# Performance work log

Measured on AMD Instinct MI355X. Metric: run time of the kernel, lower is better.

The kernel has to match this reference:

```python
import jax, jax.numpy as jnp
import numpy as np

N = 50000      # ncount
IN_CH = 256    # in_channels
OUT_CH = 128   # out_channels
NNZ = 800000   # nnz per sparse matrix (avg degree 16)


def _spmm(rows, cols, vals, dense, n_rows):
    # sparse(COO) @ dense : gather rows of dense by col index, scale, scatter-add by row
    contrib = vals[:, None] * dense[cols]              # [nnz, F]
    return jax.ops.segment_sum(contrib, rows, num_segments=n_rows)


def setup_inputs() -> dict:
    key = jax.random.key(0)
    ks = jax.random.split(key, 12)
    phi_indices = jnp.stack([
        jax.random.randint(ks[0], (NNZ,), 0, N),
        jax.random.randint(ks[1], (NNZ,), 0, N)])
    phi_values = jax.random.normal(ks[2], (NNZ,), dtype=jnp.float32)
    phi_inverse_indices = jnp.stack([
        jax.random.randint(ks[3], (NNZ,), 0, N),
        jax.random.randint(ks[4], (NNZ,), 0, N)])
    phi_inverse_values = jax.random.normal(ks[5], (NNZ,), dtype=jnp.float32)
    feature_indices = jnp.stack([
        jax.random.randint(ks[6], (NNZ,), 0, N),       # node index
        jax.random.randint(ks[7], (NNZ,), 0, IN_CH)])  # feature column
    feature_values = jax.random.normal(ks[8], (NNZ,), dtype=jnp.float32)
    # xavier_uniform for weight_matrix
    limit = float(np.sqrt(6.0 / (IN_CH + OUT_CH)))
    weight_matrix = jax.random.uniform(ks[9], (IN_CH, OUT_CH), jnp.float32, -limit, limit)
    # diagonal filter Theta init uniform(0.9, 1.1)
    diagonal_weight_filter = jax.random.uniform(ks[10], (N,), jnp.float32, 0.9, 1.1)
    return {
        "phi_indices": phi_indices,
        "phi_values": phi_values,
        "phi_inverse_indices": phi_inverse_indices,
        "phi_inverse_values": phi_inverse_values,
        "feature_indices": feature_indices,
        "feature_values": feature_values,
        "weight_matrix": weight_matrix,
        "diagonal_weight_filter": diagonal_weight_filter,
        "dropout": 0,
    }


def reference(phi_indices, phi_values, phi_inverse_indices, phi_inverse_values,
              feature_indices, feature_values, weight_matrix,
              diagonal_weight_filter, dropout):
    # rescaled_phi = phi @ diag(theta): scales column j of phi by theta[j]
    scaled_phi_vals = phi_values * diagonal_weight_filter[phi_indices[1]]
    # filtered = features(sparse N x IN) @ W  -> [N, OUT]
    filtered = _spmm(feature_indices[0], feature_indices[1], feature_values,
                     weight_matrix, N)
    # (phi * D * phi_inv) @ filtered computed associatively without dense N x N:
    tmp = _spmm(phi_inverse_indices[0], phi_inverse_indices[1],
                phi_inverse_values, filtered, N)              # phi_inv @ filtered
    localized = _spmm(phi_indices[0], phi_indices[1],
                      scaled_phi_vals, tmp, N)                # (phi D) @ tmp
    # dropout in eval mode (training=False) is identity
    return jax.nn.relu(localized)
```

## Files before the change

kernel.cpp:

```cpp
#include <hip/hip_runtime.h>
#include <hip/hip_fp16.h>


#define OUT_CH 128
#define HALF_CH 64
#define RPB 256
#define RPB_SHIFT 8
#define MAX_NB 256
#define EPB 4096
#define EPT_C 8
#define STAGE_CAP 8192


__global__ __launch_bounds__(512) void bucket_hist_kernel(
    const int* __restrict__ rows0, int n0,
    const int* __restrict__ rows1, int n1,
    const int* __restrict__ rows2, int n2,
    int* __restrict__ hist_part,
    int NB, int NBLK)
{
    int m = blockIdx.y;
    const int* rows = (m == 0) ? rows0 : (m == 1) ? rows1 : rows2;
    int nnz         = (m == 0) ? n0    : (m == 1) ? n1    : n2;
    __shared__ int bins[MAX_NB];
    int t = threadIdx.x;
    if (t < NB) bins[t] = 0;
    __syncthreads();
    int base = blockIdx.x * EPB;
    #pragma unroll
    for (int k = 0; k < EPB / 512; ++k) {
        int i = base + k * 512 + t;
        if (i < nnz) atomicAdd(&bins[rows[i] >> RPB_SHIFT], 1);
    }
    __syncthreads();
    int* out = hist_part + ((size_t)(m * NBLK + blockIdx.x)) * NB;
    if (t < NB) out[t] = bins[t];
}


__global__ __launch_bounds__(256) void reduce_totals_kernel(
    const int* __restrict__ hist_part, int* __restrict__ totals, int NB, int NBLK)
{
    int w = blockIdx.x * 4 + (threadIdx.x >> 6);
    if (w >= 3 * NB) return;
    int lane = threadIdx.x & 63;
    int m = w / NB, b = w - m * NB;
    const int* hp = hist_part + (size_t)m * NBLK * NB + b;
    int sum = 0;
    for (int blk = lane; blk < NBLK; blk += 64)
        sum += hp[(size_t)blk * NB];
    #pragma unroll
    for (int s = 1; s < 64; s <<= 1) sum += __shfl_xor(sum, s);
    if (lane == 0) totals[w] = sum;
}


__global__ __launch_bounds__(256) void scan_bases_kernel(
    const int* __restrict__ totals, int* __restrict__ bases,
    int* __restrict__ cursor, int NB)
{
    int m = blockIdx.x, t = threadIdx.x;
    int x = (t < NB) ? totals[m * NB + t] : 0;
    int lane = t & 63, wid = t >> 6;
    int incl = x;
    #pragma unroll
    for (int s = 1; s < 64; s <<= 1) {
        int y = __shfl_up(incl, s);
        if (lane >= s) incl += y;
    }
    __shared__ int wtot[4], wbase[4];
    if (lane == 63) wtot[wid] = incl;
    __syncthreads();
    if (t == 0) {
        int run = 0;
        #pragma unroll
        for (int w = 0; w < 4; ++w) { int v = wtot[w]; wbase[w] = run; run += v; }
    }
    __syncthreads();
    if (t < NB) {
        int excl = wbase[wid] + incl - x;
        bases[m * NB + t] = excl;
        cursor[m * NB + t] = excl;
    }
}


__global__ __launch_bounds__(512) void bucket_scatter_kernel(
    const int* __restrict__ rows0, const int* __restrict__ cols0, const float* __restrict__ vals0, int n0,
    const int* __restrict__ rows1, const int* __restrict__ cols1, const float* __restrict__ vals1, int n1,
    const int* __restrict__ rows2, const int* __restrict__ cols2, const float* __restrict__ vals2, int n2,
    const float* __restrict__ theta,
    const int* __restrict__ hist_part, int* __restrict__ cursor,
    int2* __restrict__ eb0, int2* __restrict__ eb1, int2* __restrict__ eb2,
    int NB, int NBLK)
{
    int m = blockIdx.y;
    const int* rows; const int* cols; const float* vals; int nnz; int2* eb;
    if (m == 0)      { rows = rows0; cols = cols0; vals = vals0; nnz = n0; eb = eb0; }
    else if (m == 1) { rows = rows1; cols = cols1; vals = vals1; nnz = n1; eb = eb1; }
    else             { rows = rows2; cols = cols2; vals = vals2; nnz = n2; eb = eb2; }

    __shared__ int2 staged[EPB];
    __shared__ unsigned char bucket_of[EPB];
    __shared__ int lstart[MAX_NB];
    __shared__ int lcur[MAX_NB];
    __shared__ int gbase[MAX_NB];
    __shared__ int wtot[8], wbase[8];

    int t = threadIdx.x;
    int base = blockIdx.x * EPB;
    bool fold = (m == 2);

    int  bk[EPT_C];
    int2 pl[EPT_C];
    #pragma unroll
    for (int k = 0; k < EPT_C; ++k) {
        int i = base + k * 512 + t;
        if (i < nnz) {
            int r = rows[i], c = cols[i];
            float v = vals[i];
            if (fold) v *= theta[c];
            bk[k] = r >> RPB_SHIFT;
            pl[k] = make_int2(c | ((r & (RPB - 1)) << 16), __float_as_int(v));
        } else bk[k] = -1;
    }

    {
        const int* hp = hist_part + ((size_t)(m * NBLK + blockIdx.x)) * NB;
        int lh = (t < NB) ? hp[t] : 0;
        int lane = t & 63, wid = t >> 6;
        int incl = lh;
        #pragma unroll
        for (int s = 1; s < 64; s <<= 1) {
            int y = __shfl_up(incl, s);
            if (lane >= s) incl += y;
        }
        if (lane == 63) wtot[wid] = incl;
        __syncthreads();
        if (t == 0) {
            int run = 0;
            #pragma unroll
            for (int w = 0; w < 8; ++w) { int v = wtot[w]; wbase[w] = run; run += v; }
        }
        __syncthreads();
        if (t < NB) {
            int excl = wbase[wid] + incl - lh;
            lstart[t] = excl;
            lcur[t]   = excl;
            gbase[t] = atomicAdd(&cursor[m * NB + t], lh);
        }
    }
    __syncthreads();

    #pragma unroll
    for (int k = 0; k < EPT_C; ++k) {
        if (bk[k] >= 0) {
            int idx = atomicAdd(&lcur[bk[k]], 1);
            staged[idx] = pl[k];
            bucket_of[idx] = (unsigned char)bk[k];
        }
    }
    __syncthreads();

    int count = min(EPB, nnz - base);
    for (int i = t; i < count; i += 512) {
        int b = bucket_of[i];
        int dest = gbase[b] + (i - lstart[b]);
        eb[dest] = staged[i];
    }
}


__global__ __launch_bounds__(512) void bucket_to_csr_kernel(
    const int2* __restrict__ eb0, const int2* __restrict__ eb1, const int2* __restrict__ eb2,
    unsigned int* __restrict__ ec0, unsigned int* __restrict__ ec1, unsigned int* __restrict__ ec2,
    const int* __restrict__ bases,
    int* __restrict__ off,
    int n0, int n1, int n2, int NB, int n)
{
    int m = blockIdx.y;
    int b = blockIdx.x;
    const int2* eb; unsigned int* ec; int nnz;
    if (m == 0)      { eb = eb0; ec = ec0; nnz = n0; }
    else if (m == 1) { eb = eb1; ec = ec1; nnz = n1; }
    else             { eb = eb2; ec = ec2; nnz = n2; }
    int base = bases[m * NB + b];
    int end  = (b + 1 < NB) ? bases[m * NB + b + 1] : nnz;
    int cnt  = end - base;

    __shared__ unsigned int staged_c[STAGE_CAP];
    __shared__ int hist[RPB];
    __shared__ int cur[RPB];
    __shared__ int loc[RPB + 1];
    __shared__ int wtot[4];
    __shared__ int wbase[4];
    int t = threadIdx.x;
    if (t < RPB) { hist[t] = 0; cur[t] = 0; }
    __syncthreads();
    for (int i = base + t; i < end; i += 512)
        atomicAdd(&hist[(eb[i].x >> 16) & (RPB - 1)], 1);
    __syncthreads();
    {
        int x = (t < RPB) ? hist[t] : 0;
        int lane = t & 63, wid = t >> 6;
        int incl = x;
        #pragma unroll
        for (int s = 1; s < 64; s <<= 1) {
            int y = __shfl_up(incl, s);
            if (lane >= s) incl += y;
        }
        if (lane == 63 && wid < 4) wtot[wid] = incl;
        __syncthreads();
        if (t == 0) {
            int run = 0;
            #pragma unroll
            for (int w = 0; w < 4; ++w) { int v = wtot[w]; wbase[w] = run; run += v; }
        }
        __syncthreads();
        if (t < RPB) {
            loc[t] = wbase[wid] + incl - x;
            if (t == RPB - 1) loc[RPB] = wbase[3] + incl;
        }
    }
    __syncthreads();
    if (t < RPB) {
        int r = b * RPB + t;
        if (r <= n) off[(size_t)m * (n + 1) + r] = base + loc[t];
        if (b == NB - 1 && t == 0) off[(size_t)m * (n + 1) + n] = nnz;
    }
    if (cnt <= STAGE_CAP) {
        for (int i = base + t; i < end; i += 512) {
            int2 e = eb[i];
            int rl = (e.x >> 16) & (RPB - 1);
            int rk = atomicAdd(&cur[rl], 1);
            unsigned short h = __half_as_ushort(__float2half_rn(__int_as_float(e.y)));
            staged_c[loc[rl] + rk] = (unsigned int)(e.x & 0xFFFF) | ((unsigned int)h << 16);
        }
        __syncthreads();
        for (int i = t; i < cnt; i += 512)
            ec[base + i] = staged_c[i];
    } else {
        for (int i = base + t; i < end; i += 512) {
            int2 e = eb[i];
            int rl = (e.x >> 16) & (RPB - 1);
            int rk = atomicAdd(&cur[rl], 1);
            unsigned short h = __half_as_ushort(__float2half_rn(__int_as_float(e.y)));
            ec[base + loc[rl] + rk] = (unsigned int)(e.x & 0xFFFF) | ((unsigned int)h << 16);
        }
    }
}


template<bool SRC_H, bool DST_H, bool RELU>
__global__ __launch_bounds__(256) void spmm_csr_kernel(
    const int* __restrict__ off, const unsigned int* __restrict__ edges,
    const void* __restrict__ dense_v, void* __restrict__ out_v, int nrows)
{
    int lane = threadIdx.x & 63;
    int r = blockIdx.x * 4 + (threadIdx.x >> 6);
    if (r >= nrows) return;
    int j   = __builtin_amdgcn_readfirstlane(off[r]);
    int end = __builtin_amdgcn_readfirstlane(off[r + 1]);
    const float2*  df = (const float2*)dense_v;
    const __half2* dh = (const __half2*)dense_v;

    float2 a0 = make_float2(0.f, 0.f), a1 = make_float2(0.f, 0.f);

    for (; j + 16 <= end; j += 16) {
        unsigned int e[16]; float2 d[16];
        #pragma unroll
        for (int k = 0; k < 16; ++k) e[k] = edges[j + k];
        #pragma unroll
        for (int k = 0; k < 16; ++k) {
            if (SRC_H) d[k] = __half22float2(dh[(size_t)(e[k] & 0xFFFF) * HALF_CH + lane]);
            else       d[k] = df[(size_t)(e[k] & 0xFFFF) * HALF_CH + lane];
        }
        #pragma unroll
        for (int k = 0; k < 16; ++k) {
            float v = __half2float(__ushort_as_half((unsigned short)(e[k] >> 16)));
            if (k & 1) { a1.x = fmaf(v, d[k].x, a1.x); a1.y = fmaf(v, d[k].y, a1.y); }
            else       { a0.x = fmaf(v, d[k].x, a0.x); a0.y = fmaf(v, d[k].y, a0.y); }
        }
    }
    for (; j + 8 <= end; j += 8) {
        unsigned int e[8]; float2 d[8];
        #pragma unroll
        for (int k = 0; k < 8; ++k) e[k] = edges[j + k];
        #pragma unroll
        for (int k = 0; k < 8; ++k) {
            if (SRC_H) d[k] = __half22float2(dh[(size_t)(e[k] & 0xFFFF) * HALF_CH + lane]);
            else       d[k] = df[(size_t)(e[k] & 0xFFFF) * HALF_CH + lane];
        }
        #pragma unroll
        for (int k = 0; k < 8; ++k) {
            float v = __half2float(__ushort_as_half((unsigned short)(e[k] >> 16)));
            if (k & 1) { a1.x = fmaf(v, d[k].x, a1.x); a1.y = fmaf(v, d[k].y, a1.y); }
            else       { a0.x = fmaf(v, d[k].x, a0.x); a0.y = fmaf(v, d[k].y, a0.y); }
        }
    }
    for (; j + 4 <= end; j += 4) {
        unsigned int e[4]; float2 d[4];
        #pragma unroll
        for (int k = 0; k < 4; ++k) e[k] = edges[j + k];
        #pragma unroll
        for (int k = 0; k < 4; ++k) {
            if (SRC_H) d[k] = __half22float2(dh[(size_t)(e[k] & 0xFFFF) * HALF_CH + lane]);
            else       d[k] = df[(size_t)(e[k] & 0xFFFF) * HALF_CH + lane];
        }
        #pragma unroll
        for (int k = 0; k < 4; ++k) {
            float v = __half2float(__ushort_as_half((unsigned short)(e[k] >> 16)));
            if (k & 1) { a1.x = fmaf(v, d[k].x, a1.x); a1.y = fmaf(v, d[k].y, a1.y); }
            else       { a0.x = fmaf(v, d[k].x, a0.x); a0.y = fmaf(v, d[k].y, a0.y); }
        }
    }
    for (; j < end; ++j) {
        unsigned int e0 = edges[j];
        float2 d0;
        if (SRC_H) d0 = __half22float2(dh[(size_t)(e0 & 0xFFFF) * HALF_CH + lane]);
        else       d0 = df[(size_t)(e0 & 0xFFFF) * HALF_CH + lane];
        float v0 = __half2float(__ushort_as_half((unsigned short)(e0 >> 16)));
        a0.x = fmaf(v0, d0.x, a0.x); a0.y = fmaf(v0, d0.y, a0.y);
    }
    float2 res = make_float2(a0.x + a1.x, a0.y + a1.y);
    if (RELU) { res.x = fmaxf(res.x, 0.f); res.y = fmaxf(res.y, 0.f); }
    if (DST_H) ((__half2*)out_v)[(size_t)r * HALF_CH + lane] = __float22half2_rn(res);
    else       ((float2*) out_v)[(size_t)r * HALF_CH + lane] = res;
}


__global__ __launch_bounds__(256) void spmm_atomic_kernel(
    const int* __restrict__ rows, const int* __restrict__ cols,
    const float* __restrict__ vals, const float* __restrict__ theta,
    const float* __restrict__ dense, float* __restrict__ out, int nnz)
{
    int idx = blockIdx.x * blockDim.x + threadIdx.x;
    int e = idx >> 7;
    int f = idx & (OUT_CH - 1);
    if (e >= nnz) return;
    int r = rows[e];
    int c = cols[e];
    float v = vals[e];
    if (theta != nullptr) v *= theta[c];
    atomicAdd(&out[(size_t)r * OUT_CH + f], v * dense[(size_t)c * OUT_CH + f]);
}

__global__ __launch_bounds__(256) void relu_kernel(float* __restrict__ out, int n4)
{
    int i = blockIdx.x * blockDim.x + threadIdx.x;
    if (i >= n4) return;
    float4 v = ((float4*)out)[i];
    v.x = fmaxf(v.x, 0.f); v.y = fmaxf(v.y, 0.f);
    v.z = fmaxf(v.z, 0.f); v.w = fmaxf(v.w, 0.f);
    ((float4*)out)[i] = v;
}


static inline size_t align16(size_t x) { return (x + 15) & ~(size_t)15; }

extern "C" void kernel_launch(void* const* d_in, const int* in_sizes, int n_in,
                              void* d_out, int out_size, void* d_ws, size_t ws_size,
                              hipStream_t stream)
{
    const int*   phi_idx   = (const int*)d_in[0];
    const float* phi_vals  = (const float*)d_in[1];
    const int*   phii_idx  = (const int*)d_in[2];
    const float* phii_vals = (const float*)d_in[3];
    const int*   feat_idx  = (const int*)d_in[4];
    const float* feat_vals = (const float*)d_in[5];
    const float* W         = (const float*)d_in[6];
    const float* theta     = (const float*)d_in[7];

    const int nnz_phi  = in_sizes[1];
    const int nnz_phii = in_sizes[3];
    const int nnz_feat = in_sizes[5];
    const int n_nodes  = in_sizes[7];
    const int in_ch    = in_sizes[6] / OUT_CH;
    const size_t dense_elems = (size_t)n_nodes * OUT_CH;
    const long long total_e = (long long)nnz_feat + nnz_phii + nnz_phi;

    const int NB = (n_nodes + RPB - 1) >> RPB_SHIFT;
    int max_nnz = nnz_feat > nnz_phii ? nnz_feat : nnz_phii;
    if (nnz_phi > max_nnz) max_nnz = nnz_phi;
    const int NBLK = (max_nnz + EPB - 1) / EPB;

    size_t p = 0;
    size_t filtered_off = p; p += align16(dense_elems * sizeof(__half));
    size_t tmp_off      = p; p += align16(dense_elems * sizeof(__half));
    size_t off_off      = p; p += align16((size_t)3 * (n_nodes + 1) * sizeof(int));
    size_t hp_off       = p; p += align16((size_t)3 * NBLK * NB * sizeof(int));
    size_t tot_off      = p; p += align16((size_t)3 * NB * sizeof(int));
    size_t bas_off      = p; p += align16((size_t)3 * NB * sizeof(int));
    size_t cur_off      = p; p += align16((size_t)3 * NB * sizeof(int));
    size_t eb_off       = p; p += align16((size_t)total_e * sizeof(int2));
    size_t ec_off       = p; p += align16((size_t)total_e * sizeof(unsigned int));
    size_t need = p;

    char* ws = (char*)d_ws;
    dim3 block256(256);
    dim3 block512(512);

    bool fast_ok = (ws_size >= need) && (NB <= MAX_NB) && (n_nodes <= 65536) &&
                   (in_ch <= 65536);

    if (fast_ok) {
        __half* filtered = (__half*)(ws + filtered_off);
        __half* tmp      = (__half*)(ws + tmp_off);
        int* off_arr    = (int*)(ws + off_off);
        int* hist_part  = (int*)(ws + hp_off);
        int* totals     = (int*)(ws + tot_off);
        int* bases      = (int*)(ws + bas_off);
        int* cursor     = (int*)(ws + cur_off);
        int2* eb0 = (int2*)(ws + eb_off);
        int2* eb1 = eb0 + nnz_feat;
        int2* eb2 = eb1 + nnz_phii;
        unsigned int* ec0 = (unsigned int*)(ws + ec_off);
        unsigned int* ec1 = ec0 + nnz_feat;
        unsigned int* ec2 = ec1 + nnz_phii;

        const int* rows0 = feat_idx;  const int* cols0 = feat_idx + nnz_feat;
        const int* rows1 = phii_idx;  const int* cols1 = phii_idx + nnz_phii;
        const int* rows2 = phi_idx;   const int* cols2 = phi_idx  + nnz_phi;

        bucket_hist_kernel<<<dim3(NBLK, 3), block512, 0, stream>>>(
            rows0, nnz_feat, rows1, nnz_phii, rows2, nnz_phi,
            hist_part, NB, NBLK);

        int nwaves = 3 * NB;
        reduce_totals_kernel<<<dim3((nwaves + 3) / 4), block256, 0, stream>>>(
            hist_part, totals, NB, NBLK);

        scan_bases_kernel<<<dim3(3), block256, 0, stream>>>(
            totals, bases, cursor, NB);

        bucket_scatter_kernel<<<dim3(NBLK, 3), block512, 0, stream>>>(
            rows0, cols0, feat_vals, nnz_feat,
            rows1, cols1, phii_vals, nnz_phii,
            rows2, cols2, phi_vals,  nnz_phi,
            theta, hist_part, cursor, eb0, eb1, eb2, NB, NBLK);

        bucket_to_csr_kernel<<<dim3(NB, 3), block512, 0, stream>>>(
            eb0, eb1, eb2, ec0, ec1, ec2, bases, off_arr,
            nnz_feat, nnz_phii, nnz_phi, NB, n_nodes);

        int* off_f  = off_arr;
        int* off_pi = off_arr + (n_nodes + 1);
        int* off_p  = off_arr + 2 * (n_nodes + 1);

        dim3 grid_r((unsigned)((n_nodes + 3) / 4));
        spmm_csr_kernel<false, true, false><<<grid_r, block256, 0, stream>>>(
            off_f,  ec0, (const void*)W, (void*)filtered, n_nodes);
        spmm_csr_kernel<true, true, false><<<grid_r, block256, 0, stream>>>(
            off_pi, ec1, (const void*)filtered, (void*)tmp, n_nodes);
        spmm_csr_kernel<true, false, true><<<grid_r, block256, 0, stream>>>(
            off_p,  ec2, (const void*)tmp, d_out, n_nodes);
    } else {
        float* filtered = (float*)ws;
        float* tmp      = filtered + dense_elems;
        hipMemsetAsync(filtered, 0, 2 * dense_elems * sizeof(float), stream);
        hipMemsetAsync(d_out, 0, (size_t)out_size * sizeof(float), stream);
        {
            long long t = (long long)nnz_feat * OUT_CH;
            spmm_atomic_kernel<<<dim3((unsigned)((t + 255) / 256)), block256, 0, stream>>>(
                feat_idx, feat_idx + nnz_feat, feat_vals, nullptr, W, filtered, nnz_feat);
        }
        {
            long long t = (long long)nnz_phii * OUT_CH;
            spmm_atomic_kernel<<<dim3((unsigned)((t + 255) / 256)), block256, 0, stream>>>(
                phii_idx, phii_idx + nnz_phii, phii_vals, nullptr, filtered, tmp, nnz_phii);
        }
        {
            long long t = (long long)nnz_phi * OUT_CH;
            spmm_atomic_kernel<<<dim3((unsigned)((t + 255) / 256)), block256, 0, stream>>>(
                phi_idx, phi_idx + nnz_phi, phi_vals, theta, tmp, (float*)d_out, nnz_phi);
        }
        {
            int n4 = out_size / 4;
            relu_kernel<<<dim3((n4 + 255) / 256), block256, 0, stream>>>((float*)d_out, n4);
        }
    }
}
```

Baseline: 209.2 us.

## Fuse bucket histogram and scatter into one block-local sort pass

Replaces the separate histogram and global-scatter kernels with a single kernel that reads the COO input once, sorts each block's edges by bucket in shared memory, and writes them contiguously along with per-block bucket offsets. The CSR builder then gathers each bucket's segments from every source block instead of reading a pre-scattered global buffer. Values are converted to half early, and metadata and values are split into separate arrays, which shrinks intermediate traffic. The cost is a second read of the input that is removed, traded against more fragmented segment reads in the CSR kernel and a new limit on the block count.

```diff
diff --git a/kernel.cpp b/kernel.cpp
--- a/kernel.cpp
+++ b/kernel.cpp
@@ -7,34 +7,102 @@
 #define RPB 256
 #define RPB_SHIFT 8
 #define MAX_NB 256
+#define MAX_NBLK 256
 #define EPB 4096
 #define EPT_C 8
 #define STAGE_CAP 8192
 
 
-__global__ __launch_bounds__(512) void bucket_hist_kernel(
-    const int* __restrict__ rows0, int n0,
-    const int* __restrict__ rows1, int n1,
-    const int* __restrict__ rows2, int n2,
+__global__ __launch_bounds__(512) void sort_local_kernel(
+    const int* __restrict__ rows0, const int* __restrict__ cols0, const float* __restrict__ vals0, int n0,
+    const int* __restrict__ rows1, const int* __restrict__ cols1, const float* __restrict__ vals1, int n1,
+    const int* __restrict__ rows2, const int* __restrict__ cols2, const float* __restrict__ vals2, int n2,
+    const float* __restrict__ theta,
     int* __restrict__ hist_part,
+    unsigned int*  __restrict__ ebm0, unsigned int*  __restrict__ ebm1, unsigned int*  __restrict__ ebm2,
+    unsigned short* __restrict__ ebv0, unsigned short* __restrict__ ebv1, unsigned short* __restrict__ ebv2,
     int NB, int NBLK)
 {
     int m = blockIdx.y;
-    const int* rows = (m == 0) ? rows0 : (m == 1) ? rows1 : rows2;
-    int nnz         = (m == 0) ? n0    : (m == 1) ? n1    : n2;
-    __shared__ int bins[MAX_NB];
+    const int* rows; const int* cols; const float* vals; int nnz;
+    unsigned int* ebm; unsigned short* ebv;
+    if (m == 0)      { rows = rows0; cols = cols0; vals = vals0; nnz = n0; ebm = ebm0; ebv = ebv0; }
+    else if (m == 1) { rows = rows1; cols = cols1; vals = vals1; nnz = n1; ebm = ebm1; ebv = ebv1; }
+    else             { rows = rows2; cols = cols2; vals = vals2; nnz = n2; ebm = ebm2; ebv = ebv2; }
+
+    __shared__ unsigned int  staged_m[EPB];
+    __shared__ unsigned short staged_v[EPB];
+    __shared__ int lhist[MAX_NB];
+    __shared__ int lcur[MAX_NB];
+    __shared__ int wtot[8], wbase[8];
+
     int t = threadIdx.x;
-    if (t < NB) bins[t] = 0;
-    __syncthreads();
     int base = blockIdx.x * EPB;
+    bool fold = (m == 2);
+
+    if (t < NB) lhist[t] = 0;
+    __syncthreads();
+
+    int bk[EPT_C];
+    unsigned int  mt[EPT_C];
+    unsigned short vl[EPT_C];
     #pragma unroll
-    for (int k = 0; k < EPB / 512; ++k) {
+    for (int k = 0; k < EPT_C; ++k) {
         int i = base + k * 512 + t;
-        if (i < nnz) atomicAdd(&bins[rows[i] >> RPB_SHIFT], 1);
-    }
-    __syncthreads();
-    int* out = hist_part + ((size_t)(m * NBLK + blockIdx.x)) * NB;
-    if (t < NB) out[t] = bins[t];
+        if (i < nnz) {
+            int r = rows[i], c = cols[i];
+            float v = vals[i];
+            if (fold) v *= theta[c];
+            bk[k] = r >> RPB_SHIFT;
+            mt[k] = (unsigned int)c | ((unsigned int)(r & (RPB - 1)) << 16);
+            vl[k] = __half_as_ushort(__float2half_rn(v));
+            atomicAdd(&lhist[bk[k]], 1);
+        } else bk[k] = -1;
+    }
+    __syncthreads();
+
+    {
+        int x = (t < NB) ? lhist[t] : 0;
+        int lane = t & 63, wid = t >> 6;
+        int incl = x;
+        #pragma unroll
+        for (int s = 1; s < 64; s <<= 1) {
+            int y = __shfl_up(incl, s);
+            if (lane >= s) incl += y;
+        }
+        if (lane == 63) wtot[wid] = incl;
+        __syncthreads();
+        if (t == 0) {
+            int run = 0;
+            #pragma unroll
+            for (int w = 0; w < 8; ++w) { int v = wtot[w]; wbase[w] = run; run += v; }
+        }
+        __syncthreads();
+        int* out = hist_part + ((size_t)(m * NBLK + blockIdx.x)) * (NB + 1);
+        if (t < NB) {
+            int excl = wbase[wid] + incl - x;
+            lcur[t] = excl;
+            out[t] = excl;
+        }
+        if (t == 0) out[NB] = min(EPB, nnz - base);
+    }
+    __syncthreads();
+
+    #pragma unroll
+    for (int k = 0; k < EPT_C; ++k) {
+        if (bk[k] >= 0) {
+            int idx = atomicAdd(&lcur[bk[k]], 1);
+            staged_m[idx] = mt[k];
+            staged_v[idx] = vl[k];
+        }
+    }
+    __syncthreads();
+
+    int count = min(EPB, nnz - base);
+    for (int i = t; i < count; i += 512) {
+        ebm[base + i] = staged_m[i];
+        ebv[base + i] = staged_v[i];
+    }
 }
 
 
@@ -45,10 +113,12 @@
     if (w >= 3 * NB) return;
     int lane = threadIdx.x & 63;
     int m = w / NB, b = w - m * NB;
-    const int* hp = hist_part + (size_t)m * NBLK * NB + b;
+    const int* hp = hist_part + (size_t)m * NBLK * (NB + 1);
     int sum = 0;
-    for (int blk = lane; blk < NBLK; blk += 64)
-        sum += hp[(size_t)blk * NB];
+    for (int blk = lane; blk < NBLK; blk += 64) {
+        const int* row = hp + (size_t)blk * (NB + 1);
+        sum += row[b + 1] - row[b];
+    }
     #pragma unroll
     for (int s = 1; s < 64; s <<= 1) sum += __shfl_xor(sum, s);
     if (lane == 0) totals[w] = sum;
@@ -56,8 +126,7 @@
 
 
 __global__ __launch_bounds__(256) void scan_bases_kernel(
-    const int* __restrict__ totals, int* __restrict__ bases,
-    int* __restrict__ cursor, int NB)
+    const int* __restrict__ totals, int* __restrict__ bases, int NB)
 {
     int m = blockIdx.x, t = threadIdx.x;
     int x = (t < NB) ? totals[m * NB + t] : 0;
@@ -77,175 +146,131 @@
         for (int w = 0; w < 4; ++w) { int v = wtot[w]; wbase[w] = run; run += v; }
     }
     __syncthreads();
-    if (t < NB) {
-        int excl = wbase[wid] + incl - x;
-        bases[m * NB + t] = excl;
-        cursor[m * NB + t] = excl;
-    }
-}
-
-
-__global__ __launch_bounds__(512) void bucket_scatter_kernel(
-    const int* __restrict__ rows0, const int* __restrict__ cols0, const float* __restrict__ vals0, int n0,
-    const int* __restrict__ rows1, const int* __restrict__ cols1, const float* __restrict__ vals1, int n1,
-    const int* __restrict__ rows2, const int* __restrict__ cols2, const float* __restrict__ vals2, int n2,
-    const float* __restrict__ theta,
-    const int* __restrict__ hist_part, int* __restrict__ cursor,
-    int2* __restrict__ eb0, int2* __restrict__ eb1, int2* __restrict__ eb2,
-    int NB, int NBLK)
+    if (t < NB) bases[m * NB + t] = wbase[wid] + incl - x;
+}
+
+
+__global__ __launch_bounds__(512) void bucket_to_csr_kernel(
+    const unsigned int* __restrict__ ebm0, const unsigned int* __restrict__ ebm1, const unsigned int* __restrict__ ebm2,
+    const unsigned short* __restrict__ ebv0, const unsigned short* __restrict__ ebv1, const unsigned short* __restrict__ ebv2,
+    unsigned int* __restrict__ ec0, unsigned int* __restrict__ ec1, unsigned int* __restrict__ ec2,
+    const int* __restrict__ hist_part, const int* __restrict__ bases,
+    int* __restrict__ off,
+    int n0, int n1, int n2, int NB, int NBLK, int n)
 {
     int m = blockIdx.y;
-    const int* rows; const int* cols; const float* vals; int nnz; int2* eb;
-    if (m == 0)      { rows = rows0; cols = cols0; vals = vals0; nnz = n0; eb = eb0; }
-    else if (m == 1) { rows = rows1; cols = cols1; vals = vals1; nnz = n1; eb = eb1; }
-    else             { rows = rows2; cols = cols2; vals = vals2; nnz = n2; eb = eb2; }
-
-    __shared__ int2 staged[EPB];
-    __shared__ unsigned char bucket_of[EPB];
-    __shared__ int lstart[MAX_NB];
-    __shared__ int lcur[MAX_NB];
-    __shared__ int gbase[MAX_NB];
-    __shared__ int wtot[8], wbase[8];
+    int b = blockIdx.x;
+    const unsigned int* ebm; const unsigned short* ebv; unsigned int* ec; int nnz;
+    if (m == 0)      { ebm = ebm0; ebv = ebv0; ec = ec0; nnz = n0; }
+    else if (m == 1) { ebm = ebm1; ebv = ebv1; ec = ec1; nnz = n1; }
+    else             { ebm = ebm2; ebv = ebv2; ec = ec2; nnz = n2; }
+
+    __shared__ unsigned int staged_c[STAGE_CAP];
+    __shared__ int segsrc[MAX_NBLK];
+    __shared__ int segstart[MAX_NBLK + 1];
+    __shared__ int hist[RPB];
+    __shared__ int cur[RPB];
+    __shared__ int loc[RPB + 1];
+    __shared__ int wtot8[8], wbase8[8];
+    __shared__ int wtot4[4], wbase4[4];
 
     int t = threadIdx.x;
-    int base = blockIdx.x * EPB;
-    bool fold = (m == 2);
-
-    int  bk[EPT_C];
-    int2 pl[EPT_C];
-    #pragma unroll
-    for (int k = 0; k < EPT_C; ++k) {
-        int i = base + k * 512 + t;
-        if (i < nnz) {
-            int r = rows[i], c = cols[i];
-            float v = vals[i];
-            if (fold) v *= theta[c];
-            bk[k] = r >> RPB_SHIFT;
-            pl[k] = make_int2(c | ((r & (RPB - 1)) << 16), __float_as_int(v));
-        } else bk[k] = -1;
-    }
-
+    int lane = t & 63, wid = t >> 6;
+
+    int slen = 0;
+    if (t < NBLK) {
+        const int* row = hist_part + ((size_t)(m * NBLK + t)) * (NB + 1);
+        int a = row[b];
+        slen = row[b + 1] - a;
+        segsrc[t] = t * EPB + a;
+    }
+    if (t < RPB) { hist[t] = 0; cur[t] = 0; }
     {
-        const int* hp = hist_part + ((size_t)(m * NBLK + blockIdx.x)) * NB;
-        int lh = (t < NB) ? hp[t] : 0;
-        int lane = t & 63, wid = t >> 6;
-        int incl = lh;
+        int incl = slen;
         #pragma unroll
         for (int s = 1; s < 64; s <<= 1) {
             int y = __shfl_up(incl, s);
             if (lane >= s) incl += y;
         }
-        if (lane == 63) wtot[wid] = incl;
+        if (lane == 63) wtot8[wid] = incl;
         __syncthreads();
         if (t == 0) {
             int run = 0;
             #pragma unroll
-            for (int w = 0; w < 8; ++w) { int v = wtot[w]; wbase[w] = run; run += v; }
-        }
-        __syncthreads();
-        if (t < NB) {
-            int excl = wbase[wid] + incl - lh;
-            lstart[t] = excl;
-            lcur[t]   = excl;
-            gbase[t] = atomicAdd(&cursor[m * NB + t], lh);
-        }
-    }
-    __syncthreads();
-
-    #pragma unroll
-    for (int k = 0; k < EPT_C; ++k) {
-        if (bk[k] >= 0) {
-            int idx = atomicAdd(&lcur[bk[k]], 1);
-            staged[idx] = pl[k];
-            bucket_of[idx] = (unsigned char)bk[k];
-        }
-    }
-    __syncthreads();
-
-    int count = min(EPB, nnz - base);
-    for (int i = t; i < count; i += 512) {
-        int b = bucket_of[i];
-        int dest = gbase[b] + (i - lstart[b]);
-        eb[dest] = staged[i];
-    }
-}
-
-
-__global__ __launch_bounds__(512) void bucket_to_csr_kernel(
-    const int2* __restrict__ eb0, const int2* __restrict__ eb1, const int2* __restrict__ eb2,
-    unsigned int* __restrict__ ec0, unsigned int* __restrict__ ec1, unsigned int* __restrict__ ec2,
-    const int* __restrict__ bases,
-    int* __restrict__ off,
-    int n0, int n1, int n2, int NB, int n)
-{
-    int m = blockIdx.y;
-    int b = blockIdx.x;
-    const int2* eb; unsigned int* ec; int nnz;
-    if (m == 0)      { eb = eb0; ec = ec0; nnz = n0; }
-    else if (m == 1) { eb = eb1; ec = ec1; nnz = n1; }
-    else             { eb = eb2; ec = ec2; nnz = n2; }
-    int base = bases[m * NB + b];
-    int end  = (b + 1 < NB) ? bases[m * NB + b + 1] : nnz;
-    int cnt  = end - base;
-
-    __shared__ unsigned int staged_c[STAGE_CAP];
-    __shared__ int hist[RPB];
-    __shared__ int cur[RPB];
-    __shared__ int loc[RPB + 1];
-    __shared__ int wtot[4];
-    __shared__ int wbase[4];
-    int t = threadIdx.x;
-    if (t < RPB) { hist[t] = 0; cur[t] = 0; }
-    __syncthreads();
-    for (int i = base + t; i < end; i += 512)
-        atomicAdd(&hist[(eb[i].x >> 16) & (RPB - 1)], 1);
-    __syncthreads();
+            for (int w = 0; w < 8; ++w) { int v = wtot8[w]; wbase8[w] = run; run += v; }
+            segstart[NBLK] = run;
+        }
+        __syncthreads();
+        if (t < NBLK) segstart[t] = wbase8[wid] + incl - slen;
+    }
+    __syncthreads();
+
+    int cnt = segstart[NBLK];
+    int base_out = bases[m * NB + b];
+
+    for (int s = wid; s < NBLK; s += 8) {
+        int len = segstart[s + 1] - segstart[s];
+        int src = segsrc[s];
+        for (int k = lane; k < len; k += 64)
+            atomicAdd(&hist[(ebm[src + k] >> 16) & (RPB - 1)], 1);
+    }
+    __syncthreads();
+
     {
         int x = (t < RPB) ? hist[t] : 0;
-        int lane = t & 63, wid = t >> 6;
         int incl = x;
         #pragma unroll
         for (int s = 1; s < 64; s <<= 1) {
             int y = __shfl_up(incl, s);
             if (lane >= s) incl += y;
         }
-        if (lane == 63 && wid < 4) wtot[wid] = incl;
+        if (lane == 63 && wid < 4) wtot4[wid] = incl;
         __syncthreads();
         if (t == 0) {
             int run = 0;
             #pragma unroll
-            for (int w = 0; w < 4; ++w) { int v = wtot[w]; wbase[w] = run; run += v; }
+            for (int w = 0; w < 4; ++w) { int v = wtot4[w]; wbase4[w] = run; run += v; }
         }
         __syncthreads();
         if (t < RPB) {
-            loc[t] = wbase[wid] + incl - x;
-            if (t == RPB - 1) loc[RPB] = wbase[3] + incl;
-        }
-    }
-    __syncthreads();
+            loc[t] = wbase4[wid] + incl - x;
+            if (t == RPB - 1) loc[RPB] = wbase4[3] + incl;
+        }
+    }
+    __syncthreads();
+
     if (t < RPB) {
         int r = b * RPB + t;
-        if (r <= n) off[(size_t)m * (n + 1) + r] = base + loc[t];
+        if (r <= n) off[(size_t)m * (n + 1) + r] = base_out + loc[t];
         if (b == NB - 1 && t == 0) off[(size_t)m * (n + 1) + n] = nnz;
     }
+
     if (cnt <= STAGE_CAP) {
-        for (int i = base + t; i < end; i += 512) {
-            int2 e = eb[i];
-            int rl = (e.x >> 16) & (RPB - 1);
-            int rk = atomicAdd(&cur[rl], 1);
-            unsigned short h = __half_as_ushort(__float2half_rn(__int_as_float(e.y)));
-            staged_c[loc[rl] + rk] = (unsigned int)(e.x & 0xFFFF) | ((unsigned int)h << 16);
+        for (int s = wid; s < NBLK; s += 8) {
+            int len = segstart[s + 1] - segstart[s];
+            int src = segsrc[s];
+            for (int k = lane; k < len; k += 64) {
+                unsigned int meta = ebm[src + k];
+                unsigned int val  = ebv[src + k];
+                int rl = (meta >> 16) & (RPB - 1);
+                int rk = atomicAdd(&cur[rl], 1);
+                staged_c[loc[rl] + rk] = (meta & 0xFFFFu) | (val << 16);
+            }
         }
         __syncthreads();
         for (int i = t; i < cnt; i += 512)
-            ec[base + i] = staged_c[i];
+            ec[base_out + i] = staged_c[i];
     } else {
-        for (int i = base + t; i < end; i += 512) {
-            int2 e = eb[i];
-            int rl = (e.x >> 16) & (RPB - 1);
-            int rk = atomicAdd(&cur[rl], 1);
-            unsigned short h = __half_as_ushort(__float2half_rn(__int_as_float(e.y)));
-            ec[base + loc[rl] + rk] = (unsigned int)(e.x & 0xFFFF) | ((unsigned int)h << 16);
+        for (int s = wid; s < NBLK; s += 8) {
+            int len = segstart[s + 1] - segstart[s];
+            int src = segsrc[s];
+            for (int k = lane; k < len; k += 64) {
+                unsigned int meta = ebm[src + k];
+                unsigned int val  = ebv[src + k];
+                int rl = (meta >> 16) & (RPB - 1);
+                int rk = atomicAdd(&cur[rl], 1);
+                ec[base_out + loc[rl] + rk] = (meta & 0xFFFFu) | (val << 16);
+            }
         }
     }
 }
@@ -384,15 +409,20 @@
     if (nnz_phi > max_nnz) max_nnz = nnz_phi;
     const int NBLK = (max_nnz + EPB - 1) / EPB;
 
+    const int nblk0 = (nnz_feat + EPB - 1) / EPB;
+    const int nblk1 = (nnz_phii + EPB - 1) / EPB;
+    const int nblk2 = (nnz_phi  + EPB - 1) / EPB;
+    const size_t ebm_elems = ((size_t)nblk0 + nblk1 + nblk2) * EPB;
+
     size_t p = 0;
     size_t filtered_off = p; p += align16(dense_elems * sizeof(__half));
     size_t tmp_off      = p; p += align16(dense_elems * sizeof(__half));
     size_t off_off      = p; p += align16((size_t)3 * (n_nodes + 1) * sizeof(int));
-    size_t hp_off       = p; p += align16((size_t)3 * NBLK * NB * sizeof(int));
+    size_t hp_off       = p; p += align16((size_t)3 * NBLK * (MAX_NB + 1) * sizeof(int));
     size_t tot_off      = p; p += align16((size_t)3 * NB * sizeof(int));
     size_t bas_off      = p; p += align16((size_t)3 * NB * sizeof(int));
-    size_t cur_off      = p; p += align16((size_t)3 * NB * sizeof(int));
-    size_t eb_off       = p; p += align16((size_t)total_e * sizeof(int2));
+    size_t ebm_off      = p; p += align16(ebm_elems * sizeof(unsigned int));
+    size_t ebv_off      = p; p += align16(ebm_elems * sizeof(unsigned short));
     size_t ec_off       = p; p += align16((size_t)total_e * sizeof(unsigned int));
     size_t need = p;
 
@@ -400,8 +430,8 @@
     dim3 block256(256);
     dim3 block512(512);
 
-    bool fast_ok = (ws_size >= need) && (NB <= MAX_NB) && (n_nodes <= 65536) &&
-                   (in_ch <= 65536);
+    bool fast_ok = (ws_size >= need) && (NB <= MAX_NB) && (NBLK <= MAX_NBLK) &&
+                   (n_nodes <= 65536) && (in_ch <= 65536);
 
     if (fast_ok) {
         __half* filtered = (__half*)(ws + filtered_off);
@@ -410,10 +440,12 @@
         int* hist_part  = (int*)(ws + hp_off);
         int* totals     = (int*)(ws + tot_off);
         int* bases      = (int*)(ws + bas_off);
-        int* cursor     = (int*)(ws + cur_off);
-        int2* eb0 = (int2*)(ws + eb_off);
-        int2* eb1 = eb0 + nnz_feat;
-        int2* eb2 = eb1 + nnz_phii;
+        unsigned int*  ebm0 = (unsigned int*)(ws + ebm_off);
+        unsigned int*  ebm1 = ebm0 + (size_t)nblk0 * EPB;
+        unsigned int*  ebm2 = ebm1 + (size_t)nblk1 * EPB;
+        unsigned short* ebv0 = (unsigned short*)(ws + ebv_off);
+        unsigned short* ebv1 = ebv0 + (size_t)nblk0 * EPB;
+        unsigned short* ebv2 = ebv1 + (size_t)nblk1 * EPB;
         unsigned int* ec0 = (unsigned int*)(ws + ec_off);
         unsigned int* ec1 = ec0 + nnz_feat;
         unsigned int* ec2 = ec1 + nnz_phii;
@@ -422,26 +454,23 @@
         const int* rows1 = phii_idx;  const int* cols1 = phii_idx + nnz_phii;
         const int* rows2 = phi_idx;   const int* cols2 = phi_idx  + nnz_phi;
 
-        bucket_hist_kernel<<<dim3(NBLK, 3), block512, 0, stream>>>(
-            rows0, nnz_feat, rows1, nnz_phii, rows2, nnz_phi,
-            hist_part, NB, NBLK);
+        sort_local_kernel<<<dim3(NBLK, 3), block512, 0, stream>>>(
+            rows0, cols0, feat_vals, nnz_feat,
+            rows1, cols1, phii_vals, nnz_phii,
+            rows2, cols2, phi_vals,  nnz_phi,
+            theta, hist_part,
+            ebm0, ebm1, ebm2, ebv0, ebv1, ebv2, NB, NBLK);
 
         int nwaves = 3 * NB;
         reduce_totals_kernel<<<dim3((nwaves + 3) / 4), block256, 0, stream>>>(
             hist_part, totals, NB, NBLK);
 
-        scan_bases_kernel<<<dim3(3), block256, 0, stream>>>(
-            totals, bases, cursor, NB);
-
-        bucket_scatter_kernel<<<dim3(NBLK, 3), block512, 0, stream>>>(
-            rows0, cols0, feat_vals, nnz_feat,
-            rows1, cols1, phii_vals, nnz_phii,
-            rows2, cols2, phi_vals,  nnz_phi,
-            theta, hist_part, cursor, eb0, eb1, eb2, NB, NBLK);
+        scan_bases_kernel<<<dim3(3), block256, 0, stream>>>(totals, bases, NB);
 
         bucket_to_csr_kernel<<<dim3(NB, 3), block512, 0, stream>>>(
-            eb0, eb1, eb2, ec0, ec1, ec2, bases, off_arr,
-            nnz_feat, nnz_phii, nnz_phi, NB, n_nodes);
+            ebm0, ebm1, ebm2, ebv0, ebv1, ebv2, ec0, ec1, ec2,
+            hist_part, bases, off_arr,
+            nnz_feat, nnz_phii, nnz_phi, NB, NBLK, n_nodes);
 
         int* off_f  = off_arr;
         int* off_pi = off_arr + (n_nodes + 1);
```

Result: slower. 213.3 us (+2.0%).
